# Kernel optimization log

Measured on AMD Instinct MI355X. Metric: run time of the kernel, lower is better.

## Reference

```python
import jax, jax.numpy as jnp
import numpy as np

N_HEADS = 16
D_HEAD = 64
IGNORE = -100000.0


def setup_inputs() -> dict:
    key = jax.random.key(0)
    ks = jax.random.split(key, 5)
    B, S, D = 2, 2048, 1024
    return {
        "residual": jax.random.normal(ks[0], (B, S, D), dtype=jnp.float32),
        "q": jax.random.normal(ks[1], (B, S, D), dtype=jnp.float32),
        "k": jax.random.normal(ks[2], (B, S, D), dtype=jnp.float32),
        "v": jax.random.normal(ks[3], (B, S, D), dtype=jnp.float32),
        "W_O": jax.random.normal(ks[4], (N_HEADS, D_HEAD, D), dtype=jnp.float32) * 0.02,
        "b_O": jnp.zeros((D,), dtype=jnp.float32),
    }


def reference(residual, q, k, v, W_O, b_O):
    B, S, _ = q.shape
    attn_scale = np.sqrt(D_HEAD).astype(np.float32)  # use_attn_scale=True
    # split heads: [..., pos, (h d)] -> [..., pos, h, d]
    qh = q.reshape(B, S, N_HEADS, D_HEAD)
    kh = k.reshape(B, S, N_HEADS, D_HEAD)
    vh = v.reshape(B, S, N_HEADS, D_HEAD)
    # scores: [..., head, query_pos, key_pos]
    scores = jnp.einsum("bqhd,bkhd->bhqk", qh, kh) / attn_scale
    causal = jnp.tril(jnp.ones((S, S), dtype=bool))
    scores = jnp.where(causal, scores, jnp.float32(IGNORE))
    pattern = jax.nn.softmax(scores, axis=-1)
    # weighted sum of values: [..., query_pos, head, d_head]
    z = jnp.einsum("bkhd,bhqk->bqhd", vh, pattern)
    out = jnp.einsum("bqhd,hdm->bqm", z, W_O) + b_O
    return (residual, out)
```

## Files before the change

### kernel.cpp

```cpp
#include <hip/hip_runtime.h>

#define B_ 2
#define S_ 2048
#define D_ 1024
#define H_ 16
#define DH_ 64
#define NP_ 2048

typedef short v8s __attribute__((ext_vector_type(8)));
typedef float v4f __attribute__((ext_vector_type(4)));
typedef float v16f __attribute__((ext_vector_type(16)));
typedef unsigned int v2u __attribute__((ext_vector_type(2)));
typedef unsigned int v4u __attribute__((ext_vector_type(4)));
typedef unsigned int uint32;

__device__ inline short f2bf(float f) {
  unsigned u = __float_as_uint(f);
  u = (u + 0x7FFFu + ((u >> 16) & 1u)) >> 16;
  return (short)u;
}

__device__ inline unsigned pk_bf16(float lo, float hi) {
  unsigned r;
  asm("v_cvt_pk_bf16_f32 %0, %1, %2" : "=v"(r) : "v"(lo), "v"(hi));
  return r;
}

__device__ inline void gll16(const void* g, void* l) {
  __builtin_amdgcn_global_load_lds(
      (const __attribute__((address_space(1))) void*)g,
      (__attribute__((address_space(3))) void*)l, 16, 0, 0);
}

__global__ __launch_bounds__(256) void cvt_all_kernel(
    const float* __restrict__ k, short* __restrict__ kb,
    const float* __restrict__ v, short* __restrict__ vt,
    const float* __restrict__ w, short* __restrict__ wt) {
  __shared__ short t[64][64 + 8];
  int bid = blockIdx.x;
  int tid = threadIdx.x;
  if (bid < 2048) {
    int i = bid * 256 + tid;
    float4 a = ((const float4*)k)[2 * i];
    float4 b = ((const float4*)k)[2 * i + 1];
    v8s o;
    o[0] = f2bf(a.x); o[1] = f2bf(a.y); o[2] = f2bf(a.z); o[3] = f2bf(a.w);
    o[4] = f2bf(b.x); o[5] = f2bf(b.y); o[6] = f2bf(b.z); o[7] = f2bf(b.w);
    ((v8s*)kb)[i] = o;
    return;
  }
  int r = tid >> 2, c16 = (tid & 3) * 16;
  if (bid < 3072) {
    int id = bid - 2048;
    int st = id & 31;
    int bh = id >> 5;
    int b = bh >> 4, h = bh & 15;
    const float* vp = v + ((size_t)(b * S_ + st * 64 + r)) * D_ + h * DH_ + c16;
    for (int i = 0; i < 16; i += 4) {
      float4 a = *(const float4*)(vp + i);
      t[r][c16 + i + 0] = f2bf(a.x);
      t[r][c16 + i + 1] = f2bf(a.y);
      t[r][c16 + i + 2] = f2bf(a.z);
      t[r][c16 + i + 3] = f2bf(a.w);
    }
    __syncthreads();
    short* op = vt + ((size_t)((b * H_ + h) * DH_ + r)) * S_ + st * 64 + c16;
    v8s o0, o1;
    for (int j = 0; j < 8; ++j) { o0[j] = t[c16 + j][r]; o1[j] = t[c16 + 8 + j][r]; }
    *(v8s*)op = o0;
    *(v8s*)(op + 8) = o1;
  } else {
    int id = bid - 3072;
    int tk = id & 15, tm = id >> 4;
    const float* wp = w + (size_t)(tk * 64 + r) * D_ + tm * 64 + c16;
    for (int i = 0; i < 16; i += 4) {
      float4 a = *(const float4*)(wp + i);
      t[r][c16 + i + 0] = f2bf(a.x);
      t[r][c16 + i + 1] = f2bf(a.y);
      t[r][c16 + i + 2] = f2bf(a.z);
      t[r][c16 + i + 3] = f2bf(a.w);
    }
    __syncthreads();
    short* op = wt + (size_t)(tm * 64 + r) * D_ + tk * 64 + c16;
    v8s o0, o1;
    for (int j = 0; j < 8; ++j) { o0[j] = t[c16 + j][r]; o1[j] = t[c16 + 8 + j][r]; }
    *(v8s*)op = o0;
    *(v8s*)(op + 8) = o1;
  }
}

template <int SPLITS>
__global__ __launch_bounds__(128, 4) void attn_kernel(
    const float* __restrict__ q, const short* __restrict__ kbf,
    const short* __restrict__ vtb, uint32* __restrict__ Opart,
    float* __restrict__ Lsum, const float* __restrict__ residual,
    float* __restrict__ res_out) {
  int bid = blockIdx.x;
  int bh = bid & 31;
  int sp, qt;
  if constexpr (SPLITS == 2) {
    sp = (bid >> 5) & 1;
    int g = (bid >> 6) & 3, j = bid >> 8;
    qt = 31 - 4 * j - ((j & 1) ? 3 - g : g);
  } else {
    sp = 0;
    int g = (bid >> 5) & 3, j = bid >> 7;
    qt = 31 - 4 * j - ((j & 1) ? 3 - g : g);
  }
  int b = bh >> 4, h = bh & 15;

  const int tt0 = (SPLITS == 2) ? sp * (qt + 1) : 0;
  const int tt1 = (SPLITS == 2) ? tt0 + qt : 2 * qt + 1;

  int tid = threadIdx.x;
  int wave = tid >> 6, lane = tid & 63;
  int l31 = lane & 31, h32 = lane >> 5;

  __shared__ short Klds[2][32][64];
  __shared__ short Vlds[2][32][64];

  const int qrow0 = qt * 64 + wave * 32;
  const int lr8 = lane >> 3;
  const int l7 = lane & 7;

  const short* kbase = kbf + (size_t)b * S_ * D_ + h * DH_ +
                       (size_t)(wave * 8 + lr8) * D_ + ((l7 ^ lr8) << 3);
  const int vq = l7 ^ lr8;
  const short* vbase = vtb + (size_t)(b * H_ + h) * DH_ * S_ +
                       (size_t)(wave * 8 + lr8 + (vq >> 2) * 32) * S_ +
                       ((vq & 3) << 3);

  v8s qf[4];
  {
    const float* qp = q + (size_t)(b * S_ + qrow0 + l31) * D_ + h * DH_ + h32 * 8;
    const float sc = 0.125f * 1.44269504f;
#pragma unroll
    for (int d4 = 0; d4 < 4; ++d4) {
      float4 x = *(const float4*)(qp + d4 * 16);
      float4 y = *(const float4*)(qp + d4 * 16 + 4);
      v8s tq;
      tq[0] = f2bf(x.x * sc); tq[1] = f2bf(x.y * sc);
      tq[2] = f2bf(x.z * sc); tq[3] = f2bf(x.w * sc);
      tq[4] = f2bf(y.x * sc); tq[5] = f2bf(y.y * sc);
      tq[6] = f2bf(y.z * sc); tq[7] = f2bf(y.w * sc);
      qf[d4] = tq;
    }
  }

  v16f O0, O1;
#pragma unroll
  for (int r = 0; r < 16; ++r) { O0[r] = 0.f; O1[r] = 0.f; }
  float L = 0.f;
  const int swz = (l31 & 7) << 3;

  auto stage = [&](int t, int buf) {
    const short* kp = kbase + (size_t)(t * 32) * D_;
    const short* vp = vbase + t * 32;
#pragma unroll
    for (int i = 0; i < 2; ++i)
      gll16(kp + (size_t)(i * 16) * D_, &Klds[buf][i * 16 + wave * 8][0]);
#pragma unroll
    for (int i = 0; i < 2; ++i)
      gll16(vp + (size_t)(i * 16) * S_, &Vlds[buf][i * 16 + wave * 8][0]);
  };

  stage(tt0, tt0 & 1);

  for (int s = tt0; s <= tt1; ++s) {
    int cur = s & 1;
    if (s < tt1) {
      stage(s + 1, cur ^ 1);
      asm volatile("s_waitcnt vmcnt(4)" ::: "memory");
    } else {
      asm volatile("s_waitcnt vmcnt(0)" ::: "memory");
    }
    __builtin_amdgcn_sched_barrier(0);
    __builtin_amdgcn_s_barrier();
    __builtin_amdgcn_sched_barrier(0);

    int kb = s * 32;
    bool fullskip = (kb > qrow0 + 31);
    if (!fullskip) {
      bool msk = (kb + 31 > qrow0);

      __builtin_amdgcn_s_setprio(1);
      v16f S0;
#pragma unroll
      for (int r = 0; r < 16; ++r) S0[r] = 0.f;
#pragma unroll
      for (int d4 = 0; d4 < 4; ++d4) {
        v8s kf = *(const v8s*)&Klds[cur][l31][(((d4 << 1) | h32) << 3) ^ swz];
        S0 = __builtin_amdgcn_mfma_f32_32x32x16_bf16(kf, qf[d4], S0, 0, 0, 0);
      }
      __builtin_amdgcn_s_setprio(0);

      int qg = qrow0 + l31;
      if (msk) {
#pragma unroll
        for (int r = 0; r < 16; ++r) {
          int kl = kb + (r & 3) + 8 * (r >> 2) + 4 * h32;
          if (kl > qg) S0[r] = -1e30f;
        }
      }

      float rs = 0.f;
      unsigned pw0[8];
#pragma unroll
      for (int r = 0; r < 16; ++r) {
        S0[r] = __builtin_amdgcn_exp2f(S0[r]);
        rs += S0[r];
      }
#pragma unroll
      for (int w = 0; w < 8; ++w) pw0[w] = pk_bf16(S0[2 * w], S0[2 * w + 1]);
      rs += __shfl_xor(rs, 32);
      L += rs;

      __builtin_amdgcn_s_setprio(1);
#pragma unroll
      for (int ks = 0; ks < 2; ++ks) {
        v2u a = __builtin_amdgcn_permlane32_swap(pw0[ks * 4 + 0], pw0[ks * 4 + 2], false, false);
        v2u c = __builtin_amdgcn_permlane32_swap(pw0[ks * 4 + 1], pw0[ks * 4 + 3], false, false);
        v4u fw; fw.x = a.x; fw.y = c.x; fw.z = a.y; fw.w = c.y;
        v8s pb = __builtin_bit_cast(v8s, fw);
        v8s vf0 = *(const v8s*)&Vlds[cur][l31][(((ks << 1) | h32) << 3) ^ swz];
        O0 = __builtin_amdgcn_mfma_f32_32x32x16_bf16(vf0, pb, O0, 0, 0, 0);
        v8s vf1 = *(const v8s*)&Vlds[cur][l31][(((4 | (ks << 1) | h32)) << 3) ^ swz];
        O1 = __builtin_amdgcn_mfma_f32_32x32x16_bf16(vf1, pb, O1, 0, 0, 0);
      }
      __builtin_amdgcn_s_setprio(0);
    }

    __builtin_amdgcn_sched_barrier(0);
    __builtin_amdgcn_s_barrier();
    __builtin_amdgcn_sched_barrier(0);
  }

  int p = bh * 64 + qt * 2 + wave;
  uint32* Op = Opart + ((size_t)(sp * NP_ + p)) * 1024;
#pragma unroll
  for (int w = 0; w < 8; ++w) {
    int dpair = 4 * (w >> 1) + (w & 1) + 2 * h32;
    Op[dpair * 32 + l31] = pk_bf16(O0[2 * w], O0[2 * w + 1]);
    Op[(16 + dpair) * 32 + l31] = pk_bf16(O1[2 * w], O1[2 * w + 1]);
  }
  if (h32 == 0) Lsum[(size_t)(sp * NP_ + p) * 32 + l31] = L;

  {
    constexpr int NBLK = (SPLITS == 2) ? 2048 : 1024;
    const float4* rs_ = (const float4*)residual;
    float4* rd_ = (float4*)res_out;
    for (size_t i = (size_t)bid * 128 + tid; i < 1048576; i += (size_t)NBLK * 128)
      rd_[i] = rs_[i];
  }
}

template <int SPLITS>
__global__ __launch_bounds__(128) void merge_kernel(
    const uint32* __restrict__ Opart, const float* __restrict__ Lsum,
    short* __restrict__ z) {
  int p = blockIdx.x;
  int tid = threadIdx.x;
  int qq = tid & 31, g = tid >> 5;

  float Lt = Lsum[(size_t)p * 32 + qq];
  if constexpr (SPLITS == 2) Lt += Lsum[((size_t)NP_ + p) * 32 + qq];
  float f = 1.f / Lt;

  __shared__ uint32 T[32][33];
#pragma unroll
  for (int j = 0; j < 8; ++j) {
    int dp = g * 8 + j;
    uint32 u0 = Opart[(size_t)p * 1024 + dp * 32 + qq];
    float lo = __uint_as_float(u0 << 16);
    float hi = __uint_as_float(u0 & 0xFFFF0000u);
    if constexpr (SPLITS == 2) {
      uint32 u1 = Opart[((size_t)NP_ + p) * 1024 + dp * 32 + qq];
      lo += __uint_as_float(u1 << 16);
      hi += __uint_as_float(u1 & 0xFFFF0000u);
    }
    T[qq][dp] = pk_bf16(lo * f, hi * f);
  }
  __syncthreads();
  int q2 = tid >> 2, c = (tid & 3) * 8;
  int srow = (p & 63) * 32 + q2;
  int b = p >> 10, h = (p >> 6) & 15;
  uint32* zp = (uint32*)z + ((size_t)(b * S_ + srow)) * (D_ / 2) + h * 32 + c;
#pragma unroll
  for (int j = 0; j < 8; ++j) zp[j] = T[q2][c + j];
}

__global__ __launch_bounds__(256) void proj_kernel(
    const short* __restrict__ z, const short* __restrict__ wt,
    const float* __restrict__ bias, float* __restrict__ out) {
  int bm = blockIdx.x, bn = blockIdx.y;
  int tid = threadIdx.x;
  int wave = tid >> 6, lane = tid & 63, lh = lane >> 4, ll = lane & 15;
  int wr = wave >> 1, wc = wave & 1;

  __shared__ short Al[2][64][64];
  __shared__ short Bl[2][128][64];

  const int r8 = lane >> 3;
  const int scol = ((lane & 7) ^ r8) << 3;

  v4f acc[2][4];
#pragma unroll
  for (int m = 0; m < 2; ++m)
#pragma unroll
    for (int n = 0; n < 4; ++n) acc[m][n] = (v4f){0.f, 0.f, 0.f, 0.f};

  auto stage = [&](int kb, int bbuf) {
#pragma unroll
    for (int i = 0; i < 2; ++i) {
      int c = wave * 2 + i;
      gll16(z + (size_t)(bm * 64 + c * 8 + r8) * D_ + kb + scol, &Al[bbuf][c * 8][0]);
    }
#pragma unroll
    for (int i = 0; i < 4; ++i) {
      int c = wave * 4 + i;
      gll16(wt + (size_t)(bn * 128 + c * 8 + r8) * D_ + kb + scol, &Bl[bbuf][c * 8][0]);
    }
  };

  stage(0, 0);
  __syncthreads();

  for (int kt = 0; kt < D_ / 64; ++kt) {
    int bbuf = kt & 1;
    if (kt + 1 < D_ / 64) stage((kt + 1) * 64, bbuf ^ 1);
    v8s af[2][2], bf[4][2];
#pragma unroll
    for (int m = 0; m < 2; ++m) {
      int row = wr * 32 + m * 16 + ll;
#pragma unroll
      for (int c = 0; c < 2; ++c)
        af[m][c] = *(const v8s*)&Al[bbuf][row][(((c << 2) | lh) ^ (ll & 7)) << 3];
    }
#pragma unroll
    for (int n = 0; n < 4; ++n) {
      int row = wc * 64 + n * 16 + ll;
#pragma unroll
      for (int c = 0; c < 2; ++c)
        bf[n][c] = *(const v8s*)&Bl[bbuf][row][(((c << 2) | lh) ^ (ll & 7)) << 3];
    }
#pragma unroll
    for (int m = 0; m < 2; ++m)
#pragma unroll
      for (int n = 0; n < 4; ++n)
#pragma unroll
        for (int c = 0; c < 2; ++c)
          acc[m][n] = __builtin_amdgcn_mfma_f32_16x16x32_bf16(af[m][c], bf[n][c], acc[m][n], 0, 0, 0);
    __syncthreads();
  }

#pragma unroll
  for (int m = 0; m < 2; ++m) {
    int gr = bm * 64 + wr * 32 + m * 16 + lh * 4;
#pragma unroll
    for (int n = 0; n < 4; ++n) {
      int gc = bn * 128 + wc * 64 + n * 16 + ll;
      float bo = bias[gc];
#pragma unroll
      for (int r = 0; r < 4; ++r)
        out[(size_t)(gr + r) * D_ + gc] = acc[m][n][r] + bo;
    }
  }
}

extern "C" void kernel_launch(void* const* d_in, const int* in_sizes, int n_in,
                              void* d_out, int out_size, void* d_ws, size_t ws_size,
                              hipStream_t stream) {
  const float* residual = (const float*)d_in[0];
  const float* q = (const float*)d_in[1];
  const float* k = (const float*)d_in[2];
  const float* v = (const float*)d_in[3];
  const float* W = (const float*)d_in[4];
  const float* bO = (const float*)d_in[5];
  float* out = (float*)d_out;

  const size_t half = (size_t)B_ * S_ * D_;
  char* ws = (char*)d_ws;
  short* kbf = (short*)ws;
  short* vtb = kbf + half;
  short* wtb = vtb + half;
  char* pbase = (char*)(wtb + (size_t)D_ * D_);
  const size_t opart_b = (size_t)NP_ * 1024 * 4;
  const size_t l_b = (size_t)NP_ * 32 * 4;
  const size_t base_b = (size_t)pbase - (size_t)ws;
  short* z = kbf;

  cvt_all_kernel<<<3328, 256, 0, stream>>>(k, kbf, v, vtb, W, wtb);

  if (ws_size >= base_b + 2 * (opart_b + l_b)) {
    uint32* Opart = (uint32*)pbase;
    float* Lsum = (float*)(pbase + 2 * opart_b);
    attn_kernel<2><<<2048, 128, 0, stream>>>(q, kbf, vtb, Opart, Lsum, residual, out);
    merge_kernel<2><<<NP_, 128, 0, stream>>>(Opart, Lsum, z);
    proj_kernel<<<dim3((B_ * S_) / 64, D_ / 128), 256, 0, stream>>>(z, wtb, bO, out + half);
  } else {
    uint32* Opart = (uint32*)pbase;
    float* Lsum = (float*)(pbase + opart_b);
    attn_kernel<1><<<1024, 128, 0, stream>>>(q, kbf, vtb, Opart, Lsum, residual, out);
    merge_kernel<1><<<NP_, 128, 0, stream>>>(Opart, Lsum, z);
    proj_kernel<<<dim3((B_ * S_) / 64, D_ / 128), 256, 0, stream>>>(z, wtb, bO, out + half);
  }
}
```

Baseline: 76.59 us.

## Split attention blocks to one wave per 32-row query tile, single-buffered

Each attention block now has one wave handling a 32-row query tile, replacing two waves covering 64 rows. This doubles the block count and drops the LDS double buffer and the block-wide barriers. The causal split now divides the exact key-tile range per tile, so tiles lying entirely above the diagonal are no longer loaded and skipped. The cost is serialised load and compute inside each wave, since the next tile's stage is only issued after the current compute finishes, and each K/V tile is loaded by one wave only instead of being shared across two.

```diff
diff --git a/kernel.cpp b/kernel.cpp
--- a/kernel.cpp
+++ b/kernel.cpp
@@ -11,7 +11,6 @@
 typedef float v4f __attribute__((ext_vector_type(4)));
 typedef float v16f __attribute__((ext_vector_type(16)));
 typedef unsigned int v2u __attribute__((ext_vector_type(2)));
-typedef unsigned int v4u __attribute__((ext_vector_type(4)));
 typedef unsigned int uint32;
 
 __device__ inline short f2bf(float f) {
@@ -90,45 +89,37 @@
 }
 
 template <int SPLITS>
-__global__ __launch_bounds__(128, 4) void attn_kernel(
+__global__ __launch_bounds__(64, 4) void attn_kernel(
     const float* __restrict__ q, const short* __restrict__ kbf,
     const short* __restrict__ vtb, uint32* __restrict__ Opart,
     float* __restrict__ Lsum, const float* __restrict__ residual,
     float* __restrict__ res_out) {
+  constexpr int NBLK = (SPLITS == 2) ? 4096 : 2048;
   int bid = blockIdx.x;
   int bh = bid & 31;
-  int sp, qt;
-  if constexpr (SPLITS == 2) {
-    sp = (bid >> 5) & 1;
-    int g = (bid >> 6) & 3, j = bid >> 8;
-    qt = 31 - 4 * j - ((j & 1) ? 3 - g : g);
-  } else {
-    sp = 0;
-    int g = (bid >> 5) & 3, j = bid >> 7;
-    qt = 31 - 4 * j - ((j & 1) ? 3 - g : g);
-  }
+  int rest = bid >> 5;
+  int sp = (SPLITS == 2) ? (rest & 1) : 0;
+  int i = (SPLITS == 2) ? (rest >> 1) : rest;
   int b = bh >> 4, h = bh & 15;
 
-  const int tt0 = (SPLITS == 2) ? sp * (qt + 1) : 0;
-  const int tt1 = (SPLITS == 2) ? tt0 + qt : 2 * qt + 1;
-
-  int tid = threadIdx.x;
-  int wave = tid >> 6, lane = tid & 63;
+  const int qrow0 = i * 32;
+  const int nt = i + 1;
+  const int t0 = (SPLITS == 2) ? sp * nt / 2 : 0;
+  const int t1 = (SPLITS == 2) ? ((sp + 1) * nt / 2 - 1) : i;
+
+  int lane = threadIdx.x;
   int l31 = lane & 31, h32 = lane >> 5;
 
-  __shared__ short Klds[2][32][64];
-  __shared__ short Vlds[2][32][64];
-
-  const int qrow0 = qt * 64 + wave * 32;
+  __shared__ short Klds[32][64];
+  __shared__ short Vlds[32][64];
+
   const int lr8 = lane >> 3;
   const int l7 = lane & 7;
-
   const short* kbase = kbf + (size_t)b * S_ * D_ + h * DH_ +
-                       (size_t)(wave * 8 + lr8) * D_ + ((l7 ^ lr8) << 3);
+                       (size_t)lr8 * D_ + ((l7 ^ lr8) << 3);
   const int vq = l7 ^ lr8;
   const short* vbase = vtb + (size_t)(b * H_ + h) * DH_ * S_ +
-                       (size_t)(wave * 8 + lr8 + (vq >> 2) * 32) * S_ +
-                       ((vq & 3) << 3);
+                       (size_t)(lr8 + (vq >> 2) * 32) * S_ + ((vq & 3) << 3);
 
   v8s qf[4];
   {
@@ -153,89 +144,78 @@
   float L = 0.f;
   const int swz = (l31 & 7) << 3;
 
-  auto stage = [&](int t, int buf) {
+  auto stage = [&](int t) {
     const short* kp = kbase + (size_t)(t * 32) * D_;
     const short* vp = vbase + t * 32;
 #pragma unroll
-    for (int i = 0; i < 2; ++i)
-      gll16(kp + (size_t)(i * 16) * D_, &Klds[buf][i * 16 + wave * 8][0]);
-#pragma unroll
-    for (int i = 0; i < 2; ++i)
-      gll16(vp + (size_t)(i * 16) * S_, &Vlds[buf][i * 16 + wave * 8][0]);
+    for (int j = 0; j < 4; ++j)
+      gll16(kp + (size_t)(j * 8) * D_, &Klds[j * 8][0]);
+#pragma unroll
+    for (int j = 0; j < 4; ++j)
+      gll16(vp + (size_t)(j * 8) * S_, &Vlds[j * 8][0]);
   };
 
-  stage(tt0, tt0 & 1);
-
-  for (int s = tt0; s <= tt1; ++s) {
-    int cur = s & 1;
-    if (s < tt1) {
-      stage(s + 1, cur ^ 1);
-      asm volatile("s_waitcnt vmcnt(4)" ::: "memory");
-    } else {
-      asm volatile("s_waitcnt vmcnt(0)" ::: "memory");
-    }
+  if (t0 <= t1) stage(t0);
+
+  for (int s = t0; s <= t1; ++s) {
+    asm volatile("s_waitcnt vmcnt(0)" ::: "memory");
     __builtin_amdgcn_sched_barrier(0);
-    __builtin_amdgcn_s_barrier();
+
+    int kb = s * 32;
+
+    __builtin_amdgcn_s_setprio(1);
+    v16f S0;
+#pragma unroll
+    for (int r = 0; r < 16; ++r) S0[r] = 0.f;
+#pragma unroll
+    for (int d4 = 0; d4 < 4; ++d4) {
+      v8s kf = *(const v8s*)&Klds[l31][(((d4 << 1) | h32) << 3) ^ swz];
+      S0 = __builtin_amdgcn_mfma_f32_32x32x16_bf16(kf, qf[d4], S0, 0, 0, 0);
+    }
+    __builtin_amdgcn_s_setprio(0);
+
+    if (kb + 31 > qrow0) {
+      int qg = qrow0 + l31;
+#pragma unroll
+      for (int r = 0; r < 16; ++r) {
+        int kl = kb + (r & 3) + 8 * (r >> 2) + 4 * h32;
+        if (kl > qg) S0[r] = -1e30f;
+      }
+    }
+
+    float rs = 0.f;
+    unsigned pw0[8];
+#pragma unroll
+    for (int r = 0; r < 16; ++r) {
+      S0[r] = __builtin_amdgcn_exp2f(S0[r]);
+      rs += S0[r];
+    }
+#pragma unroll
+    for (int w = 0; w < 8; ++w) pw0[w] = pk_bf16(S0[2 * w], S0[2 * w + 1]);
+    rs += __shfl_xor(rs, 32);
+    L += rs;
+
+    __builtin_amdgcn_s_setprio(1);
+#pragma unroll
+    for (int ks = 0; ks < 2; ++ks) {
+      v2u a = __builtin_amdgcn_permlane32_swap(pw0[ks * 4 + 0], pw0[ks * 4 + 2], false, false);
+      v2u c = __builtin_amdgcn_permlane32_swap(pw0[ks * 4 + 1], pw0[ks * 4 + 3], false, false);
+      uint32 fw[4] = {a.x, c.x, a.y, c.y};
+      v8s pb = __builtin_bit_cast(v8s, *(ulonglong2*)fw);
+      v8s vf0 = *(const v8s*)&Vlds[l31][(((ks << 1) | h32) << 3) ^ swz];
+      O0 = __builtin_amdgcn_mfma_f32_32x32x16_bf16(vf0, pb, O0, 0, 0, 0);
+      v8s vf1 = *(const v8s*)&Vlds[l31][((4 | (ks << 1) | h32) << 3) ^ swz];
+      O1 = __builtin_amdgcn_mfma_f32_32x32x16_bf16(vf1, pb, O1, 0, 0, 0);
+    }
+    __builtin_amdgcn_s_setprio(0);
+
     __builtin_amdgcn_sched_barrier(0);
-
-    int kb = s * 32;
-    bool fullskip = (kb > qrow0 + 31);
-    if (!fullskip) {
-      bool msk = (kb + 31 > qrow0);
-
-      __builtin_amdgcn_s_setprio(1);
-      v16f S0;
-#pragma unroll
-      for (int r = 0; r < 16; ++r) S0[r] = 0.f;
-#pragma unroll
-      for (int d4 = 0; d4 < 4; ++d4) {
-        v8s kf = *(const v8s*)&Klds[cur][l31][(((d4 << 1) | h32) << 3) ^ swz];
-        S0 = __builtin_amdgcn_mfma_f32_32x32x16_bf16(kf, qf[d4], S0, 0, 0, 0);
-      }
-      __builtin_amdgcn_s_setprio(0);
-
-      int qg = qrow0 + l31;
-      if (msk) {
-#pragma unroll
-        for (int r = 0; r < 16; ++r) {
-          int kl = kb + (r & 3) + 8 * (r >> 2) + 4 * h32;
-          if (kl > qg) S0[r] = -1e30f;
-        }
-      }
-
-      float rs = 0.f;
-      unsigned pw0[8];
-#pragma unroll
-      for (int r = 0; r < 16; ++r) {
-        S0[r] = __builtin_amdgcn_exp2f(S0[r]);
-        rs += S0[r];
-      }
-#pragma unroll
-      for (int w = 0; w < 8; ++w) pw0[w] = pk_bf16(S0[2 * w], S0[2 * w + 1]);
-      rs += __shfl_xor(rs, 32);
-      L += rs;
-
-      __builtin_amdgcn_s_setprio(1);
-#pragma unroll
-      for (int ks = 0; ks < 2; ++ks) {
-        v2u a = __builtin_amdgcn_permlane32_swap(pw0[ks * 4 + 0], pw0[ks * 4 + 2], false, false);
-        v2u c = __builtin_amdgcn_permlane32_swap(pw0[ks * 4 + 1], pw0[ks * 4 + 3], false, false);
-        v4u fw; fw.x = a.x; fw.y = c.x; fw.z = a.y; fw.w = c.y;
-        v8s pb = __builtin_bit_cast(v8s, fw);
-        v8s vf0 = *(const v8s*)&Vlds[cur][l31][(((ks << 1) | h32) << 3) ^ swz];
-        O0 = __builtin_amdgcn_mfma_f32_32x32x16_bf16(vf0, pb, O0, 0, 0, 0);
-        v8s vf1 = *(const v8s*)&Vlds[cur][l31][(((4 | (ks << 1) | h32)) << 3) ^ swz];
-        O1 = __builtin_amdgcn_mfma_f32_32x32x16_bf16(vf1, pb, O1, 0, 0, 0);
-      }
-      __builtin_amdgcn_s_setprio(0);
-    }
-
+    asm volatile("s_waitcnt lgkmcnt(0)" ::: "memory");
     __builtin_amdgcn_sched_barrier(0);
-    __builtin_amdgcn_s_barrier();
-    __builtin_amdgcn_sched_barrier(0);
-  }
-
-  int p = bh * 64 + qt * 2 + wave;
+    if (s < t1) stage(s + 1);
+  }
+
+  int p = bh * 64 + i;
   uint32* Op = Opart + ((size_t)(sp * NP_ + p)) * 1024;
 #pragma unroll
   for (int w = 0; w < 8; ++w) {
@@ -246,11 +226,11 @@
   if (h32 == 0) Lsum[(size_t)(sp * NP_ + p) * 32 + l31] = L;
 
   {
-    constexpr int NBLK = (SPLITS == 2) ? 2048 : 1024;
     const float4* rs_ = (const float4*)residual;
     float4* rd_ = (float4*)res_out;
-    for (size_t i = (size_t)bid * 128 + tid; i < 1048576; i += (size_t)NBLK * 128)
-      rd_[i] = rs_[i];
+    for (size_t idx = (size_t)bid * 64 + lane; idx < 1048576;
+         idx += (size_t)NBLK * 64)
+      rd_[idx] = rs_[idx];
   }
 }
 
@@ -394,13 +374,13 @@
   if (ws_size >= base_b + 2 * (opart_b + l_b)) {
     uint32* Opart = (uint32*)pbase;
     float* Lsum = (float*)(pbase + 2 * opart_b);
-    attn_kernel<2><<<2048, 128, 0, stream>>>(q, kbf, vtb, Opart, Lsum, residual, out);
+    attn_kernel<2><<<4096, 64, 0, stream>>>(q, kbf, vtb, Opart, Lsum, residual, out);
     merge_kernel<2><<<NP_, 128, 0, stream>>>(Opart, Lsum, z);
     proj_kernel<<<dim3((B_ * S_) / 64, D_ / 128), 256, 0, stream>>>(z, wtb, bO, out + half);
   } else {
     uint32* Opart = (uint32*)pbase;
     float* Lsum = (float*)(pbase + opart_b);
-    attn_kernel<1><<<1024, 128, 0, stream>>>(q, kbf, vtb, Opart, Lsum, residual, out);
+    attn_kernel<1><<<2048, 64, 0, stream>>>(q, kbf, vtb, Opart, Lsum, residual, out);
     merge_kernel<1><<<NP_, 128, 0, stream>>>(Opart, Lsum, z);
     proj_kernel<<<dim3((B_ * S_) / 64, D_ / 128), 256, 0, stream>>>(z, wtb, bO, out + half);
   }
```

New measurement: 83.19 us. 8.6% more time.
